# Kernel tuning notes

Hardware: AMD Instinct MI355X
Metric: run time of the kernel (lower is better)

The kernel has to match this reference:

```python
import jax, jax.numpy as jnp
import numpy as np

N = 10000      # num nodes
D = 256        # embedding dim (in_channels)
Q = 4096       # num query edges
P = 0.003      # edge density (~30 avg degree)


def setup_inputs() -> dict:
    key = jax.random.key(0)
    k1, k2, k3 = jax.random.split(key, 3)
    emb_weight = jax.random.normal(k1, (N, D), dtype=jnp.float32)
    # 0/1 dense adjacency standing in for the SparseTensor adj
    adj = (jax.random.uniform(k2, (N, N)) < P).astype(jnp.float32)
    edges = jax.random.randint(k3, (2, Q), 0, N, dtype=jnp.int64)
    return {"emb_weight": emb_weight, "adj": adj, "edges": edges}


def reference(emb_weight, adj, edges):
    # model_type='simplecos', x=None -> x = emb.weight
    x = emb_weight
    degrees = adj.sum(-1) + 1e-6                      # [N]
    # x = x + (adj @ x) / degrees[:, None]  (torch precedence: matmul then div)
    x = x + (adj @ x) / degrees[:, None]              # [N, D]
    # cosine_similarity with eps=1e-8 (torch default)
    nrm = jnp.sqrt(jnp.sum(x * x, axis=1))            # [N]
    xn = x / jnp.maximum(nrm, 1e-8)[:, None]          # [N, D]
    # common neighbors: elementwise product of adjacency rows of the two endpoints
    src, dst = edges[0], edges[1]
    cn = adj[src] * adj[dst]                          # [Q, N]
    mask = (cn != 0).astype(x.dtype)                  # [Q, N] indicator of common neighbor
    # cos(x[src[e]], x[c]) and cos(x[dst[e]], x[c]) for every candidate neighbor c
    cosL = xn[src] @ xn.T                             # [Q, N]
    cosR = xn[dst] @ xn.T                             # [Q, N]
    # sparse segment-sum over common-neighbor columns
    weights = jnp.sum(mask * cosL * cosR, axis=1)     # [Q]
    return jax.nn.sigmoid(weights)
```

## Files before the change

### kernel.cpp

```cpp
#include <hip/hip_runtime.h>
#include <math.h>

#define NN 10000
#define DD 256
#define QQ 4096
#define CAP 128


__global__ __launch_bounds__(256) void build_rows(
    const float* __restrict__ emb, const float* __restrict__ adj,
    float* __restrict__ xn, int* __restrict__ cnt, int* __restrict__ nbr)
{
    const int i = blockIdx.x;
    const int t = threadIdx.x;
    __shared__ int   s_cnt;
    __shared__ int   s_list[CAP];
    __shared__ float s_red[4];
    __shared__ float s_norm;

    if (t == 0) s_cnt = 0;
    __syncthreads();

    const float4* row = (const float4*)(adj + (size_t)i * NN);
    for (int k = t; k < NN / 4; k += 256) {
        float4 v = row[k];
        int base = k * 4;
        if (v.x != 0.f) { int p = atomicAdd(&s_cnt, 1); if (p < CAP) s_list[p] = base;     }
        if (v.y != 0.f) { int p = atomicAdd(&s_cnt, 1); if (p < CAP) s_list[p] = base + 1; }
        if (v.z != 0.f) { int p = atomicAdd(&s_cnt, 1); if (p < CAP) s_list[p] = base + 2; }
        if (v.w != 0.f) { int p = atomicAdd(&s_cnt, 1); if (p < CAP) s_list[p] = base + 3; }
    }
    __syncthreads();

    const int c = s_cnt;
    const int m = (c < CAP) ? c : CAP;

    float acc = 0.f;
    for (int k = 0; k < m; ++k)
        acc += emb[(size_t)s_list[k] * DD + t];

    const float deg = (float)c + 1e-6f;
    const float x = emb[(size_t)i * DD + t] + acc / deg;

    float s = x * x;
    #pragma unroll
    for (int o = 32; o > 0; o >>= 1) s += __shfl_down(s, o, 64);
    const int lane = t & 63, wv = t >> 6;
    if (lane == 0) s_red[wv] = s;
    __syncthreads();
    if (t == 0) {
        float tot = s_red[0] + s_red[1] + s_red[2] + s_red[3];
        s_norm = fmaxf(sqrtf(tot), 1e-8f);
    }
    __syncthreads();

    xn[(size_t)i * DD + t] = x / s_norm;

    if (t == 0) cnt[i] = m;
    for (int k = t; k < m; k += 256) nbr[(size_t)i * CAP + k] = s_list[k];
}

__global__ __launch_bounds__(256) void edge_weights(
    const int* __restrict__ edges, const float* __restrict__ xn,
    const int* __restrict__ cnt, const int* __restrict__ nbr,
    float* __restrict__ out)
{
    const int e = blockIdx.x;
    const int t = threadIdx.x;
    const int srcI = edges[e];
    const int dstI = edges[QQ + e];

    __shared__ int   s_dst[CAP];
    __shared__ int   s_com[CAP];
    __shared__ int   s_ncom;
    __shared__ float s_red[8];
    __shared__ float s_w;

    const int cs = cnt[srcI];
    const int cd = cnt[dstI];
    if (t == 0) { s_ncom = 0; s_w = 0.f; }
    for (int k = t; k < cd; k += 256) s_dst[k] = nbr[(size_t)dstI * CAP + k];
    __syncthreads();

    for (int k = t; k < cs; k += 256) {
        int a = nbr[(size_t)srcI * CAP + k];
        bool found = false;
        for (int j = 0; j < cd; ++j) { if (s_dst[j] == a) { found = true; break; } }
        if (found) { int p = atomicAdd(&s_ncom, 1); s_com[p] = a; }
    }
    __syncthreads();

    const int nc = s_ncom;
    const float vs = xn[(size_t)srcI * DD + t];
    const float vd = xn[(size_t)dstI * DD + t];
    const int lane = t & 63, wv = t >> 6;

    for (int k = 0; k < nc; ++k) {
        const float vc = xn[(size_t)s_com[k] * DD + t];
        float a = vs * vc;
        float b = vd * vc;
        #pragma unroll
        for (int o = 32; o > 0; o >>= 1) {
            a += __shfl_down(a, o, 64);
            b += __shfl_down(b, o, 64);
        }
        if (lane == 0) { s_red[wv] = a; s_red[4 + wv] = b; }
        __syncthreads();
        if (t == 0) {
            float sa = s_red[0] + s_red[1] + s_red[2] + s_red[3];
            float sb = s_red[4] + s_red[5] + s_red[6] + s_red[7];
            s_w += sa * sb;
        }
        __syncthreads();
    }

    if (t == 0) out[e] = 1.f / (1.f + expf(-s_w));
}

extern "C" void kernel_launch(void* const* d_in, const int* in_sizes, int n_in,
                              void* d_out, int out_size, void* d_ws, size_t ws_size,
                              hipStream_t stream) {
    const float* emb   = (const float*)d_in[0];
    const float* adj   = (const float*)d_in[1];
    const int*   edges = (const int*)d_in[2];
    float*       out   = (float*)d_out;

    float* xn  = (float*)d_ws;
    int*   cnt = (int*)(xn + (size_t)NN * DD);
    int*   nbr = cnt + NN;

    build_rows<<<NN, 256, 0, stream>>>(emb, adj, xn, cnt, nbr);
    edge_weights<<<QQ, 256, 0, stream>>>(edges, xn, cnt, nbr, out);
}
```

Baseline: 553.9 us.

## Batch adjacency loads, unroll neighbor gather, use one-wavefront edge blocks

In build_rows, all ten float4 adjacency loads per thread are issued before the nonzero scan, and the neighbor embedding gather uses eight independent accumulators to raise memory-level parallelism. edge_weights now runs as a single 64-lane wavefront per edge with float4 row loads and xor-shuffle reductions, which removes the per-neighbor __syncthreads and shared-memory reduction. It also returns early with sigmoid(0) when an edge has no common neighbors. The costs are extra registers for the buffered loads and fewer threads per edge doing the membership search.

```diff
diff --git a/kernel.cpp b/kernel.cpp
--- a/kernel.cpp
+++ b/kernel.cpp
@@ -22,9 +22,16 @@
     __syncthreads();
 
     const float4* row = (const float4*)(adj + (size_t)i * NN);
-    for (int k = t; k < NN / 4; k += 256) {
-        float4 v = row[k];
-        int base = k * 4;
+    float4 r[10];
+    #pragma unroll
+    for (int j = 0; j < 10; ++j) {
+        int k = t + j * 256;
+        r[j] = (k < NN / 4) ? row[k] : make_float4(0.f, 0.f, 0.f, 0.f);
+    }
+    #pragma unroll
+    for (int j = 0; j < 10; ++j) {
+        float4 v = r[j];
+        int base = (t + j * 256) * 4;
         if (v.x != 0.f) { int p = atomicAdd(&s_cnt, 1); if (p < CAP) s_list[p] = base;     }
         if (v.y != 0.f) { int p = atomicAdd(&s_cnt, 1); if (p < CAP) s_list[p] = base + 1; }
         if (v.z != 0.f) { int p = atomicAdd(&s_cnt, 1); if (p < CAP) s_list[p] = base + 2; }
@@ -35,9 +42,18 @@
     const int c = s_cnt;
     const int m = (c < CAP) ? c : CAP;
 
-    float acc = 0.f;
-    for (int k = 0; k < m; ++k)
-        acc += emb[(size_t)s_list[k] * DD + t];
+    float a0=0.f,a1=0.f,a2=0.f,a3=0.f,a4=0.f,a5=0.f,a6=0.f,a7=0.f;
+    int k = 0;
+    for (; k + 8 <= m; k += 8) {
+        int i0=s_list[k],   i1=s_list[k+1], i2=s_list[k+2], i3=s_list[k+3];
+        int i4=s_list[k+4], i5=s_list[k+5], i6=s_list[k+6], i7=s_list[k+7];
+        a0 += emb[(size_t)i0*DD + t]; a1 += emb[(size_t)i1*DD + t];
+        a2 += emb[(size_t)i2*DD + t]; a3 += emb[(size_t)i3*DD + t];
+        a4 += emb[(size_t)i4*DD + t]; a5 += emb[(size_t)i5*DD + t];
+        a6 += emb[(size_t)i6*DD + t]; a7 += emb[(size_t)i7*DD + t];
+    }
+    for (; k < m; ++k) a0 += emb[(size_t)s_list[k]*DD + t];
+    const float acc = ((a0+a1)+(a2+a3)) + ((a4+a5)+(a6+a7));
 
     const float deg = (float)c + 1e-6f;
     const float x = emb[(size_t)i * DD + t] + acc / deg;
@@ -57,33 +73,31 @@
     xn[(size_t)i * DD + t] = x / s_norm;
 
     if (t == 0) cnt[i] = m;
-    for (int k = t; k < m; k += 256) nbr[(size_t)i * CAP + k] = s_list[k];
+    for (int q = t; q < m; q += 256) nbr[(size_t)i * CAP + q] = s_list[q];
 }
 
-__global__ __launch_bounds__(256) void edge_weights(
+__global__ __launch_bounds__(64) void edge_weights(
     const int* __restrict__ edges, const float* __restrict__ xn,
     const int* __restrict__ cnt, const int* __restrict__ nbr,
     float* __restrict__ out)
 {
     const int e = blockIdx.x;
-    const int t = threadIdx.x;
+    const int lane = threadIdx.x;
     const int srcI = edges[e];
     const int dstI = edges[QQ + e];
 
-    __shared__ int   s_dst[CAP];
-    __shared__ int   s_com[CAP];
-    __shared__ int   s_ncom;
-    __shared__ float s_red[8];
-    __shared__ float s_w;
+    __shared__ int s_dst[CAP];
+    __shared__ int s_com[CAP];
+    __shared__ int s_ncom;
 
     const int cs = cnt[srcI];
     const int cd = cnt[dstI];
-    if (t == 0) { s_ncom = 0; s_w = 0.f; }
-    for (int k = t; k < cd; k += 256) s_dst[k] = nbr[(size_t)dstI * CAP + k];
+    if (lane == 0) s_ncom = 0;
+    for (int q = lane; q < cd; q += 64) s_dst[q] = nbr[(size_t)dstI * CAP + q];
     __syncthreads();
 
-    for (int k = t; k < cs; k += 256) {
-        int a = nbr[(size_t)srcI * CAP + k];
+    for (int q = lane; q < cs; q += 64) {
+        int a = nbr[(size_t)srcI * CAP + q];
         bool found = false;
         for (int j = 0; j < cd; ++j) { if (s_dst[j] == a) { found = true; break; } }
         if (found) { int p = atomicAdd(&s_ncom, 1); s_com[p] = a; }
@@ -91,30 +105,24 @@
     __syncthreads();
 
     const int nc = s_ncom;
-    const float vs = xn[(size_t)srcI * DD + t];
-    const float vd = xn[(size_t)dstI * DD + t];
-    const int lane = t & 63, wv = t >> 6;
+    if (nc == 0) { if (lane == 0) out[e] = 0.5f; return; }
 
-    for (int k = 0; k < nc; ++k) {
-        const float vc = xn[(size_t)s_com[k] * DD + t];
-        float a = vs * vc;
-        float b = vd * vc;
+    const float4 vs = ((const float4*)(xn + (size_t)srcI * DD))[lane];
+    const float4 vd = ((const float4*)(xn + (size_t)dstI * DD))[lane];
+
+    float w = 0.f;
+    for (int q = 0; q < nc; ++q) {
+        const float4 vc = ((const float4*)(xn + (size_t)s_com[q] * DD))[lane];
+        float a = vs.x*vc.x + vs.y*vc.y + vs.z*vc.z + vs.w*vc.w;
+        float b = vd.x*vc.x + vd.y*vc.y + vd.z*vc.z + vd.w*vc.w;
         #pragma unroll
         for (int o = 32; o > 0; o >>= 1) {
-            a += __shfl_down(a, o, 64);
-            b += __shfl_down(b, o, 64);
+            a += __shfl_xor(a, o, 64);
+            b += __shfl_xor(b, o, 64);
         }
-        if (lane == 0) { s_red[wv] = a; s_red[4 + wv] = b; }
-        __syncthreads();
-        if (t == 0) {
-            float sa = s_red[0] + s_red[1] + s_red[2] + s_red[3];
-            float sb = s_red[4] + s_red[5] + s_red[6] + s_red[7];
-            s_w += sa * sb;
-        }
-        __syncthreads();
+        w += a * b;
     }
-
-    if (t == 0) out[e] = 1.f / (1.f + expf(-s_w));
+    if (lane == 0) out[e] = 1.f / (1.f + expf(-w));
 }
 
 extern "C" void kernel_launch(void* const* d_in, const int* in_sizes, int n_in,
@@ -130,5 +138,5 @@
     int*   nbr = cnt + NN;
 
     build_rows<<<NN, 256, 0, stream>>>(emb, adj, xn, cnt, nbr);
-    edge_weights<<<QQ, 256, 0, stream>>>(edges, xn, cnt, nbr, out);
+    edge_weights<<<QQ, 64, 0, stream>>>(edges, xn, cnt, nbr, out);
 }
```

Measured after the change: 542.1 us. -2.1%, faster.
